# Kernel optimization log

Measured on AMD Instinct MI355X. Metric: run time of the kernel, lower is better.

## Reference

```python
import jax, jax.numpy as jnp
import numpy as np

L, D, H, DFF = 4, 1024, 16, 4096
DH = D // H
B, T = 2, 2048
EPS = 1e-5


def setup_inputs() -> dict:
    key = jax.random.key(0)
    ks = jax.random.split(key, 16)
    xav_a = (6.0 / (D + D)) ** 0.5      # xavier_uniform for square DxD
    xav_f1 = (6.0 / (D + DFF)) ** 0.5
    xav_f2 = (6.0 / (DFF + D)) ** 0.5
    def u(k, shape, a):
        return jax.random.uniform(k, shape, jnp.float32, -a, a)
    inp = {
        "x": jax.random.normal(ks[0], (B, T, D), jnp.float32),
        "mask": jnp.ones((B, T), jnp.int32),
        # attention projections, torch Linear layout [out, in]
        "Wq": u(ks[1], (L, D, D), xav_a), "bq": jnp.zeros((L, D), jnp.float32),
        "Wk": u(ks[2], (L, D, D), xav_a), "bk": jnp.zeros((L, D), jnp.float32),
        "Wv": u(ks[3], (L, D, D), xav_a), "bv": jnp.zeros((L, D), jnp.float32),
        "Wo": u(ks[4], (L, D, D), xav_a), "bo": jnp.zeros((L, D), jnp.float32),
        # FFN
        "fc1_w": u(ks[5], (L, DFF, D), xav_f1), "fc1_b": jnp.zeros((L, DFF), jnp.float32),
        "fc2_w": u(ks[6], (L, D, DFF), xav_f2), "fc2_b": jnp.zeros((L, D), jnp.float32),
        # LayerNorms
        "ln1_g": jnp.ones((L, D), jnp.float32), "ln1_b": jnp.zeros((L, D), jnp.float32),
        "ln2_g": jnp.ones((L, D), jnp.float32), "ln2_b": jnp.zeros((L, D), jnp.float32),
        "lnf_g": jnp.ones((D,), jnp.float32), "lnf_b": jnp.zeros((D,), jnp.float32),
    }
    return inp


def _layernorm(x, g, b):
    mu = jnp.mean(x, axis=-1, keepdims=True)
    var = jnp.mean(jnp.square(x - mu), axis=-1, keepdims=True)
    return (x - mu) * jax.lax.rsqrt(var + EPS) * g + b


def _encoder_forward(x, mask, Wq, bq, Wk, bk, Wv, bv, Wo, bo,
                     fc1_w, fc1_b, fc2_w, fc2_b,
                     ln1_g, ln1_b, ln2_g, ln2_b, lnf_g, lnf_b):
    keep = mask.astype(bool)[:, None, None, :]  # [B,1,1,Tk]
    scale = 1.0 / (DH ** 0.5)
    for l in range(L):
        # --- multi-head self-attention ---
        q = (jnp.einsum('btd,ed->bte', x, Wq[l]) + bq[l]).reshape(B, T, H, DH).transpose(0, 2, 1, 3)
        k = (jnp.einsum('btd,ed->bte', x, Wk[l]) + bk[l]).reshape(B, T, H, DH).transpose(0, 2, 1, 3)
        v = (jnp.einsum('btd,ed->bte', x, Wv[l]) + bv[l]).reshape(B, T, H, DH).transpose(0, 2, 1, 3)
        logits = jnp.einsum('bhqd,bhkd->bhqk', q, k) * scale
        logits = jnp.where(keep, logits, -jnp.inf)
        attn = jax.nn.softmax(logits, axis=-1)
        ctx = jnp.einsum('bhqk,bhkd->bhqd', attn, v).transpose(0, 2, 1, 3).reshape(B, T, D)
        attn_out = jnp.einsum('btd,ed->bte', ctx, Wo[l]) + bo[l]
        x = _layernorm(x + attn_out, ln1_g[l], ln1_b[l])
        # --- feed-forward (exact GELU, like torch nn.GELU default) ---
        h = jax.nn.gelu(jnp.einsum('btd,fd->btf', x, fc1_w[l]) + fc1_b[l], approximate=False)
        ff_out = jnp.einsum('btf,df->btd', h, fc2_w[l]) + fc2_b[l]
        x = _layernorm(x + ff_out, ln2_g[l], ln2_b[l])
    return _layernorm(x, lnf_g, lnf_b)


def reference(x, mask, Wq, bq, Wk, bk, Wv, bv, Wo, bo,
              fc1_w, fc1_b, fc2_w, fc2_b,
              ln1_g, ln1_b, ln2_g, ln2_b, lnf_g, lnf_b):
    return _encoder_forward(x, mask, Wq, bq, Wk, bk, Wv, bv, Wo, bo,
                            fc1_w, fc1_b, fc2_w, fc2_b,
                            ln1_g, ln1_b, ln2_g, ln2_b, lnf_g, lnf_b)
```

## Files before the change

kernel.cpp:

```cpp
#include <hip/hip_runtime.h>
#include <hip/hip_bf16.h>
#include <cstdint>

#define BB 2
#define TT 2048
#define DD 1024
#define HH 16
#define DHH 64
#define DFF 4096
#define LL 4
#define MM (BB*TT)
#define NT (TT/64)

typedef __attribute__((ext_vector_type(8))) short short8v;
typedef __attribute__((ext_vector_type(4))) short short4v;
typedef __attribute__((ext_vector_type(4))) float floatx4;

typedef __attribute__((address_space(3))) void lds_void;
typedef const __attribute__((address_space(1))) void glb_void;

__device__ __forceinline__ void gload_lds16(const void* g, void* l) {
  __builtin_amdgcn_global_load_lds((glb_void*)g, (lds_void*)l, 16, 0, 0);
}

__device__ __forceinline__ float bf2f(short s) {
  union { unsigned u; float f; } v; v.u = ((unsigned)(unsigned short)s) << 16; return v.f;
}
__device__ __forceinline__ short f2bf(float f) {
  union { float f; unsigned u; } v; v.f = f;
  unsigned r = (v.u + 0x7fffu + ((v.u >> 16) & 1u)) >> 16;
  return (short)r;
}
__device__ __forceinline__ unsigned pack2bf(float a, float b) {
  __hip_bfloat162 h = __float22bfloat162_rn(make_float2(a, b));
  return *reinterpret_cast<unsigned*>(&h);
}
__device__ __forceinline__ float fexp2(float x) {
  float r; asm("v_exp_f32 %0, %1" : "=v"(r) : "v"(x)); return r;
}
__device__ __forceinline__ float max3f(float a, float b, float c) {
  float r; asm("v_max3_f32 %0, %1, %2, %3" : "=v"(r) : "v"(a), "v"(b), "v"(c)); return r;
}
__device__ __forceinline__ float gelu_fast(float x) {
  const float u = x * x;
  const float w = fmaf(u, -0.10294537f, -2.302203f);
  const float t = fexp2(w * x);
  return x * __builtin_amdgcn_rcpf(1.f + t);
}

#define SCL2 0.18033688011112042f
__device__ __forceinline__ short8v scale8(short8v v) {
  short8v r;
#pragma unroll
  for (int i = 0; i < 8; ++i) r[i] = f2bf(bf2f(v[i]) * SCL2);
  return r;
}

#define SEG (DD*DD)
#define WTOT (4*SEG + 2*DFF*DD)
__global__ __launch_bounds__(256) void cast_layer(
    const float* __restrict__ wq, const float* __restrict__ wk,
    const float* __restrict__ wv, const float* __restrict__ wo,
    const float* __restrict__ f1, const float* __restrict__ f2,
    short* __restrict__ dst)
{
  const int i = (blockIdx.x * 256 + threadIdx.x) * 4;
  const float* src; int off;
  if      (i <     SEG) { src = wq; off = i; }
  else if (i < 2 * SEG) { src = wk; off = i - SEG; }
  else if (i < 3 * SEG) { src = wv; off = i - 2 * SEG; }
  else if (i < 4 * SEG) { src = wo; off = i - 3 * SEG; }
  else if (i < 4 * SEG + DFF * DD) { src = f1; off = i - 4 * SEG; }
  else { src = f2; off = i - 4 * SEG - DFF * DD; }
  const float4 v = *(const float4*)(src + off);
  short4v o; o[0] = f2bf(v.x); o[1] = f2bf(v.y); o[2] = f2bf(v.z); o[3] = f2bf(v.w);
  *(short4v*)(dst + i) = o;
}

template<int GELU, int QKV>
__global__ __launch_bounds__(512, 2) void gemm256(
    const short* __restrict__ A, const short* __restrict__ W,
    const float* __restrict__ b0, const float* __restrict__ b1,
    const float* __restrict__ b2, short* __restrict__ C,
    int M, int N, int K)
{
  __shared__ __align__(16) short lds[65536];
  const int t = threadIdx.x;
  const int lane = t & 63, wave = t >> 6;
  const int wm = wave >> 2, wn = wave & 3;
  const int l15 = lane & 15, lg = lane >> 4;

  const int nwg = gridDim.x * gridDim.y;
  const int bid0 = blockIdx.y * gridDim.x + blockIdx.x;
  const int q8 = nwg >> 3;
  const int lid = (bid0 & 7) * q8 + (bid0 >> 3);
  const int bx = lid % gridDim.x, by = lid / gridDim.x;

  const size_t abase = (size_t)by * 256 * K;
  const size_t wbase = (size_t)bx * 256 * K;

  floatx4 acc[8][4];
  floatx4 zero = {0.f, 0.f, 0.f, 0.f};
#pragma unroll
  for (int m = 0; m < 8; ++m)
#pragma unroll
    for (int n = 0; n < 4; ++n) acc[m][n] = zero;

#define STG_A(sl_, h_, u_) do {                                                \
    _Pragma("unroll")                                                          \
    for (int j_ = 0; j_ < 2; ++j_) {                                           \
      const int c_ = j_ * 512 + t, r_ = c_ >> 3;                               \
      const int kc_ = (c_ & 7) ^ (r_ & 7);                                     \
      gload_lds16(A + abase + (size_t)((h_) * 128 + r_) * K + (u_) * 64 + kc_ * 8, \
                  &lds[(sl_) * 16384 + (h_) * 8192 + (j_ * 512 + wave * 64) * 8]); \
    } } while (0)
#define STG_B(sl_, h_, u_) do {                                                \
    _Pragma("unroll")                                                          \
    for (int j_ = 0; j_ < 2; ++j_) {                                           \
      const int c_ = j_ * 512 + t, r_ = c_ >> 3;                               \
      const int kc_ = (c_ & 7) ^ (r_ & 7);                                     \
      gload_lds16(W + wbase + (size_t)((h_) * 128 + r_) * K + (u_) * 64 + kc_ * 8, \
                  &lds[32768 + (sl_) * 16384 + (h_) * 8192 + (j_ * 512 + wave * 64) * 8]); \
    } } while (0)

  const int NTK = K >> 6;
  STG_A(0, 0, 0); STG_A(0, 1, 0); STG_B(0, 0, 0); STG_B(0, 1, 0);

  for (int u = 0; u < NTK; ++u) {
    const int sl = u & 1, ns = sl ^ 1;
    const int aoff = sl * 16384 + wm * 8192;
    const int boff = 32768 + sl * 16384 + (wn >> 1) * 8192;
    short8v bfr[4][2];
#pragma unroll
    for (int p = 0; p < 4; ++p) {
      if (p == 0) {
        if (u + 1 < NTK) {
          STG_A(ns, 0, u + 1);
          asm volatile("s_waitcnt vmcnt(2)" ::: "memory");
        } else {
          asm volatile("s_waitcnt vmcnt(0)" ::: "memory");
        }
        __builtin_amdgcn_s_barrier();
#pragma unroll
        for (int n = 0; n < 4; ++n)
#pragma unroll
          for (int kk = 0; kk < 2; ++kk) {
            const int rl = (wn & 1) * 64 + n * 16 + l15;
            bfr[n][kk] = *(const short8v*)&lds[boff + rl * 64 + ((kk * 4 + lg) ^ (rl & 7)) * 8];
          }
      } else if (p == 1) { if (u + 1 < NTK) STG_A(ns, 1, u + 1); }
      else if (p == 2)   { if (u + 1 < NTK) STG_B(ns, 0, u + 1); }
      else               { if (u + 1 < NTK) STG_B(ns, 1, u + 1); }

      short8v af[2][2];
#pragma unroll
      for (int i = 0; i < 2; ++i)
#pragma unroll
        for (int kk = 0; kk < 2; ++kk) {
          const int rl = (2 * p + i) * 16 + l15;
          af[i][kk] = *(const short8v*)&lds[aoff + rl * 64 + ((kk * 4 + lg) ^ (rl & 7)) * 8];
        }
      asm volatile("s_waitcnt lgkmcnt(0)" ::: "memory");
      __builtin_amdgcn_s_setprio(1);
#pragma unroll
      for (int kk = 0; kk < 2; ++kk)
#pragma unroll
        for (int i = 0; i < 2; ++i)
#pragma unroll
          for (int n = 0; n < 4; ++n)
            acc[2 * p + i][n] = __builtin_amdgcn_mfma_f32_16x16x32_bf16(
                af[i][kk], bfr[n][kk], acc[2 * p + i][n], 0, 0, 0);
      __builtin_amdgcn_s_setprio(0);
      __builtin_amdgcn_s_barrier();
    }
  }
#undef STG_A
#undef STG_B

  const float* bp;
  int cbase = bx * 256 + wn * 64;
  if (QKV) {
    const int seg = cbase >> 10;
    bp = (seg == 0) ? b0 : (seg == 1 ? b1 : b2);
    cbase -= seg << 10;
  } else {
    bp = b0;
  }
  float bv[4];
#pragma unroll
  for (int n = 0; n < 4; ++n)
    bv[n] = bp[cbase + n * 16 + l15];
#pragma unroll
  for (int m = 0; m < 8; ++m)
#pragma unroll
    for (int jj = 0; jj < 4; ++jj) {
      const int row = by * 256 + wm * 128 + m * 16 + lg * 4 + jj;
      short* cp = C + (size_t)row * N + bx * 256 + wn * 64 + l15;
#pragma unroll
      for (int n = 0; n < 4; ++n) {
        float v = acc[m][n][jj] + bv[n];
        if (GELU) v = gelu_fast(v);
        cp[n * 16] = f2bf(v);
      }
    }
}

template<int GELU>
__global__ __launch_bounds__(512, 2) void gemm128(
    const short* __restrict__ A, const short* __restrict__ W,
    const float* __restrict__ bias, short* __restrict__ C,
    int M, int N, int K)
{
  __shared__ __align__(16) short lds[49152];
  const int t = threadIdx.x;
  const int lane = t & 63, wave = t >> 6;
  const int wm = wave >> 2, wn = wave & 3;
  const int l15 = lane & 15, lg = lane >> 4;

  const int nwg = gridDim.x * gridDim.y;
  const int bid0 = blockIdx.y * gridDim.x + blockIdx.x;
  const int q8 = nwg >> 3;
  const int lid = (bid0 & 7) * q8 + (bid0 >> 3);
  const int bx = lid % gridDim.x, by = lid / gridDim.x;

  const size_t abase = (size_t)by * 128 * K;
  const size_t wbase = (size_t)bx * 128 * K;

  floatx4 acc[4][2];
  floatx4 zero = {0.f, 0.f, 0.f, 0.f};
#pragma unroll
  for (int m = 0; m < 4; ++m)
#pragma unroll
    for (int n = 0; n < 2; ++n) acc[m][n] = zero;

#define STG128(sl_, u_) do {                                                   \
    _Pragma("unroll")                                                          \
    for (int j_ = 0; j_ < 2; ++j_) {                                           \
      const int c_ = j_ * 512 + t, r_ = c_ >> 3;                               \
      const int kc_ = (c_ & 7) ^ (r_ & 7);                                     \
      gload_lds16(A + abase + (size_t)r_ * K + (u_) * 64 + kc_ * 8,            \
                  &lds[(sl_) * 8192 + (j_ * 512 + wave * 64) * 8]);            \
      gload_lds16(W + wbase + (size_t)r_ * K + (u_) * 64 + kc_ * 8,            \
                  &lds[24576 + (sl_) * 8192 + (j_ * 512 + wave * 64) * 8]);    \
    } } while (0)

  const int NTK = K >> 6;
  STG128(0, 0);
  STG128(1, 1);

  for (int u = 0; u < NTK; ++u) {
    const int sl = u % 3;
    if (u + 1 < NTK) asm volatile("s_waitcnt vmcnt(4)" ::: "memory");
    else             asm volatile("s_waitcnt vmcnt(0)" ::: "memory");
    __builtin_amdgcn_s_barrier();
    if (u + 2 < NTK) STG128((u + 2) % 3, u + 2);

    short8v bfr[2][2], af[4][2];
#pragma unroll
    for (int n = 0; n < 2; ++n)
#pragma unroll
      for (int kk = 0; kk < 2; ++kk) {
        const int rl = wn * 32 + n * 16 + l15;
        bfr[n][kk] = *(const short8v*)&lds[24576 + sl * 8192 + rl * 64 + ((kk * 4 + lg) ^ (rl & 7)) * 8];
      }
#pragma unroll
    for (int m = 0; m < 4; ++m)
#pragma unroll
      for (int kk = 0; kk < 2; ++kk) {
        const int rl = wm * 32 + ((m & 1) * 16) + l15 + (m >> 1) * 64;
        af[m][kk] = *(const short8v*)&lds[sl * 8192 + rl * 64 + ((kk * 4 + lg) ^ (rl & 7)) * 8];
      }
    asm volatile("s_waitcnt lgkmcnt(0)" ::: "memory");
    __builtin_amdgcn_s_setprio(1);
#pragma unroll
    for (int kk = 0; kk < 2; ++kk)
#pragma unroll
      for (int m = 0; m < 4; ++m)
#pragma unroll
        for (int n = 0; n < 2; ++n)
          acc[m][n] = __builtin_amdgcn_mfma_f32_16x16x32_bf16(af[m][kk], bfr[n][kk], acc[m][n], 0, 0, 0);
    __builtin_amdgcn_s_setprio(0);
  }
#undef STG128

  float bv[2];
#pragma unroll
  for (int n = 0; n < 2; ++n)
    bv[n] = bias[bx * 128 + wn * 32 + n * 16 + l15];
#pragma unroll
  for (int m = 0; m < 4; ++m)
#pragma unroll
    for (int jj = 0; jj < 4; ++jj) {
      const int row = by * 128 + wm * 32 + (m & 1) * 16 + (m >> 1) * 64 + lg * 4 + jj;
      short* cp = C + (size_t)row * N + bx * 128 + wn * 32 + l15;
#pragma unroll
      for (int n = 0; n < 2; ++n) {
        float v = acc[m][n][jj] + bv[n];
        if (GELU) v = gelu_fast(v);
        cp[n * 16] = f2bf(v);
      }
    }
}

__global__ __launch_bounds__(256) void transpose_v(
    const short* __restrict__ qkv, short* __restrict__ vt)
{
  __shared__ short tile[64][65];
  const int tb = blockIdx.x, h = blockIdx.y, b = blockIdx.z;
  const int t = threadIdx.x;
  const int r = t >> 2, c4 = (t & 3) * 16;
  const short* src = qkv + ((size_t)(b * TT + tb * 64 + r)) * 3072 + 2048 + h * 64 + c4;
#pragma unroll
  for (int i = 0; i < 16; ++i) tile[r][c4 + i] = src[i];
  __syncthreads();
  short* dst = vt + ((size_t)((b * HH + h) * 64 + r)) * TT + tb * 64 + c4;
#pragma unroll
  for (int i = 0; i < 16; ++i) dst[i] = tile[c4 + i][r];
}

#define PSTR 72
__global__ __launch_bounds__(512, 4) void flash_attn(
    const short* __restrict__ qkv, const short* __restrict__ vt,
    const int* __restrict__ mask, short* __restrict__ ctx)
{
  const int t = threadIdx.x;
  const int lane = t & 63, wave = t >> 6;
  const int l15 = lane & 15, lg = lane >> 4;

  const int bid0 = blockIdx.x + gridDim.x * (blockIdx.y + gridDim.y * blockIdx.z);
  const int lid = (bid0 & 7) * 64 + (bid0 >> 3);
  const int qb = lid & 15, h = (lid >> 4) & 15, b = lid >> 8;

  __shared__ __align__(16) short Ks[3][64 * 64];
  __shared__ __align__(16) short Vs[3][64 * 64];
  __shared__ __align__(16) short p_lds[8][16 * PSTR];
  short* prow = p_lds[wave];

  const short* qp = qkv + ((size_t)(b * TT + qb * 128 + wave * 16 + l15)) * 3072 + h * 64;
  const short8v qf0 = scale8(*(const short8v*)(qp + lg * 8));
  const short8v qf1 = scale8(*(const short8v*)(qp + 32 + lg * 8));

  const short* kbase = qkv + (size_t)b * TT * 3072 + 1024 + h * 64;
  const short* vtb   = vt + ((size_t)(b * HH + h)) * 64 * TT;

  const int srow = lane >> 3;
  const int scol = (lane & 7) ^ (srow & 7);

  float m_run = -3e30f, l_run = 0.f;
  floatx4 zero = {0.f, 0.f, 0.f, 0.f};
  floatx4 o[4];
#pragma unroll
  for (int n = 0; n < 4; ++n) o[n] = zero;

#define STAGE_KV(bufi, kb_) do {                                             \
    const int r_ = wave * 8 + srow;                                          \
    gload_lds16(kbase + (size_t)((kb_) * 64 + r_) * 3072 + scol * 8,         \
                &Ks[bufi][wave * 512]);                                      \
    gload_lds16(vtb + (size_t)r_ * TT + (kb_) * 64 + scol * 8,               \
                &Vs[bufi][wave * 512]);                                      \
  } while (0)

  STAGE_KV(0, 0);
  STAGE_KV(1, 1);
  for (int kb = 0; kb < NT; ++kb) {
    const int sl = kb % 3;
    if (kb + 1 < NT) asm volatile("s_waitcnt vmcnt(2)" ::: "memory");
    else             asm volatile("s_waitcnt vmcnt(0)" ::: "memory");
    __builtin_amdgcn_s_barrier();
    if (kb + 2 < NT) STAGE_KV((kb + 2) % 3, kb + 2);

    float cm[4][4];
#pragma unroll
    for (int n = 0; n < 4; ++n) {
      const int4 mv = *(const int4*)&mask[b * TT + kb * 64 + n * 16 + lg * 4];
      cm[n][0] = mv.x ? 0.f : -1.5e30f; cm[n][1] = mv.y ? 0.f : -1.5e30f;
      cm[n][2] = mv.z ? 0.f : -1.5e30f; cm[n][3] = mv.w ? 0.f : -1.5e30f;
    }

    floatx4 s[4];
#pragma unroll
    for (int n = 0; n < 4; ++n) {
      const int row = n * 16 + l15;
      const int ch0 = lg ^ (row & 7);
      const int ch1 = (lg + 4) ^ (row & 7);
      const short8v kf0 = *(const short8v*)&Ks[sl][row * 64 + ch0 * 8];
      const short8v kf1 = *(const short8v*)&Ks[sl][row * 64 + ch1 * 8];
      floatx4 a = zero;
      a = __builtin_amdgcn_mfma_f32_16x16x32_bf16(kf0, qf0, a, 0, 0, 0);
      a = __builtin_amdgcn_mfma_f32_16x16x32_bf16(kf1, qf1, a, 0, 0, 0);
      s[n] = a;
    }
#pragma unroll
    for (int n = 0; n < 4; ++n)
#pragma unroll
      for (int jj = 0; jj < 4; ++jj) s[n][jj] += cm[n][jj];

    const float t0 = max3f(s[0][0], s[0][1], s[0][2]);
    const float t1 = max3f(s[0][3], s[1][0], s[1][1]);
    const float t2 = max3f(s[1][2], s[1][3], s[2][0]);
    const float t3 = max3f(s[2][1], s[2][2], s[2][3]);
    const float t4 = max3f(s[3][0], s[3][1], s[3][2]);
    float mx = fmaxf(max3f(t0, t1, t2), max3f(t3, t4, s[3][3]));
    mx = fmaxf(mx, __shfl_xor(mx, 16, 64));
    mx = fmaxf(mx, __shfl_xor(mx, 32, 64));

    const bool defer = __all(mx - m_run <= 11.5f);
    const float mnew = defer ? m_run : fmaxf(m_run, mx);
    float ps[4];
#pragma unroll
    for (int n = 0; n < 4; ++n) {
      s[n][0] = fexp2(s[n][0] - mnew);
      s[n][1] = fexp2(s[n][1] - mnew);
      s[n][2] = fexp2(s[n][2] - mnew);
      s[n][3] = fexp2(s[n][3] - mnew);
      ps[n] = (s[n][0] + s[n][1]) + (s[n][2] + s[n][3]);
    }
    float sum = (ps[0] + ps[1]) + (ps[2] + ps[3]);
    sum += __shfl_xor(sum, 16, 64);
    sum += __shfl_xor(sum, 32, 64);
    if (defer) {
      l_run += sum;
    } else {
      const float al = fexp2(m_run - mnew);
      l_run = l_run * al + sum;
      m_run = mnew;
      float alo[4];
#pragma unroll
      for (int jj = 0; jj < 4; ++jj) alo[jj] = __shfl(al, lg * 4 + jj, 16);
#pragma unroll
      for (int n = 0; n < 4; ++n)
#pragma unroll
        for (int jj = 0; jj < 4; ++jj) o[n][jj] *= alo[jj];
    }

#pragma unroll
    for (int n = 0; n < 4; ++n) {
      const unsigned u0 = pack2bf(s[n][0], s[n][1]);
      const unsigned u1 = pack2bf(s[n][2], s[n][3]);
      *(uint2*)&prow[l15 * PSTR + n * 16 + lg * 4] = make_uint2(u0, u1);
    }
    const short8v pf0 = *(const short8v*)&prow[l15 * PSTR + lg * 8];
    const short8v pf1 = *(const short8v*)&prow[l15 * PSTR + 32 + lg * 8];

#pragma unroll
    for (int n = 0; n < 4; ++n) {
      const int row = n * 16 + l15;
      const int ch0 = lg ^ (row & 7);
      const int ch1 = (lg + 4) ^ (row & 7);
      const short8v vf0 = *(const short8v*)&Vs[sl][row * 64 + ch0 * 8];
      const short8v vf1 = *(const short8v*)&Vs[sl][row * 64 + ch1 * 8];
      o[n] = __builtin_amdgcn_mfma_f32_16x16x32_bf16(pf0, vf0, o[n], 0, 0, 0);
      o[n] = __builtin_amdgcn_mfma_f32_16x16x32_bf16(pf1, vf1, o[n], 0, 0, 0);
    }
  }
#undef STAGE_KV

#pragma unroll
  for (int jj = 0; jj < 4; ++jj) {
    const float inv = 1.f / __shfl(l_run, lg * 4 + jj, 16);
    const int row = qb * 128 + wave * 16 + lg * 4 + jj;
#pragma unroll
    for (int n = 0; n < 4; ++n)
      ctx[((size_t)(b * TT + row)) * DD + h * 64 + n * 16 + l15] = f2bf(o[n][jj] * inv);
  }
}

__global__ __launch_bounds__(256) void add_ln(
    const float* __restrict__ xres, const short* __restrict__ add,
    const float* __restrict__ g, const float* __restrict__ bb,
    float* __restrict__ outf, short* __restrict__ outb)
{
  const int row = blockIdx.x, t = threadIdx.x;
  const int lane = t & 63, wave = t >> 6;
  const float4 xv = *(const float4*)(xres + (size_t)row * DD + t * 4);
  float y[4] = { xv.x, xv.y, xv.z, xv.w };
  if (add) {
    const short4v av = *(const short4v*)(add + (size_t)row * DD + t * 4);
#pragma unroll
    for (int i = 0; i < 4; ++i) y[i] += bf2f(av[i]);
  }
  float s = y[0] + y[1] + y[2] + y[3];
  float ss = y[0]*y[0] + y[1]*y[1] + y[2]*y[2] + y[3]*y[3];
#pragma unroll
  for (int off = 32; off >= 1; off >>= 1) {
    s  += __shfl_xor(s, off, 64);
    ss += __shfl_xor(ss, off, 64);
  }
  __shared__ float red[2][4];
  if (lane == 0) { red[0][wave] = s; red[1][wave] = ss; }
  __syncthreads();
  s  = red[0][0] + red[0][1] + red[0][2] + red[0][3];
  ss = red[1][0] + red[1][1] + red[1][2] + red[1][3];
  const float mu = s * (1.f / DD);
  const float var = ss * (1.f / DD) - mu * mu;
  const float rs = rsqrtf(var + 1e-5f);
  const float4 gv = *(const float4*)(g + t * 4);
  const float4 bv = *(const float4*)(bb + t * 4);
  float o[4];
  o[0] = (y[0] - mu) * rs * gv.x + bv.x;
  o[1] = (y[1] - mu) * rs * gv.y + bv.y;
  o[2] = (y[2] - mu) * rs * gv.z + bv.z;
  o[3] = (y[3] - mu) * rs * gv.w + bv.w;
  if (outf) *(float4*)(outf + (size_t)row * DD + t * 4) = make_float4(o[0], o[1], o[2], o[3]);
  if (outb) {
    short4v ov;
#pragma unroll
    for (int i = 0; i < 4; ++i) ov[i] = f2bf(o[i]);
    *(short4v*)(outb + (size_t)row * DD + t * 4) = ov;
  }
}

__global__ __launch_bounds__(256) void cast_in(
    const float* __restrict__ x, float* __restrict__ xf,
    short* __restrict__ xb)
{
  const int i = (blockIdx.x * 256 + threadIdx.x) * 4;
  const float4 v = *(const float4*)(x + i);
  *(float4*)(xf + i) = v;
  short4v o; o[0] = f2bf(v.x); o[1] = f2bf(v.y); o[2] = f2bf(v.z); o[3] = f2bf(v.w);
  *(short4v*)(xb + i) = o;
}

extern "C" void kernel_launch(void* const* d_in, const int* in_sizes, int n_in,
                              void* d_out, int out_size, void* d_ws, size_t ws_size,
                              hipStream_t stream) {
  const float* x   = (const float*)d_in[0];
  const int* mask  = (const int*)d_in[1];
  const float* Wq  = (const float*)d_in[2];
  const float* bq  = (const float*)d_in[3];
  const float* Wk  = (const float*)d_in[4];
  const float* bk  = (const float*)d_in[5];
  const float* Wv  = (const float*)d_in[6];
  const float* bv  = (const float*)d_in[7];
  const float* Wo  = (const float*)d_in[8];
  const float* bo  = (const float*)d_in[9];
  const float* f1w = (const float*)d_in[10];
  const float* f1b = (const float*)d_in[11];
  const float* f2w = (const float*)d_in[12];
  const float* f2b = (const float*)d_in[13];
  const float* l1g = (const float*)d_in[14];
  const float* l1b = (const float*)d_in[15];
  const float* l2g = (const float*)d_in[16];
  const float* l2b = (const float*)d_in[17];
  const float* lfg = (const float*)d_in[18];
  const float* lfb = (const float*)d_in[19];
  float* out = (float*)d_out;

  char* ws = (char*)d_ws;
  const size_t MB = 1u << 20;
  float* xf   = (float*)(ws);
  short* xb   = (short*)(ws + 16 * MB);
  short* qkv  = (short*)(ws + 24 * MB);
  short* vt_  = (short*)(ws + 48 * MB);
  short* ctx  = (short*)(ws + 56 * MB);
  short* tmp  = (short*)(ws + 64 * MB);
  short* wbuf = (short*)(ws + 72 * MB);
  short* hb   = qkv;

  cast_in<<<(MM * DD) / (256 * 4), 256, 0, stream>>>(x, xf, xb);

  for (int l = 0; l < LL; ++l) {
    cast_layer<<<WTOT / (256 * 4), 256, 0, stream>>>(
        Wq + (size_t)l * SEG, Wk + (size_t)l * SEG, Wv + (size_t)l * SEG, Wo + (size_t)l * SEG,
        f1w + (size_t)l * DFF * DD, f2w + (size_t)l * DD * DFF, wbuf);
    const short* wqkv_b = wbuf;
    const short* wo_b   = wbuf + 3 * SEG;
    const short* f1_b   = wbuf + 4 * SEG;
    const short* f2_b   = wbuf + 4 * SEG + DFF * DD;

    gemm256<0,1><<<dim3(3072 / 256, MM / 256), 512, 0, stream>>>(
        xb, wqkv_b, bq + l * DD, bk + l * DD, bv + l * DD, qkv, MM, 3072, DD);
    transpose_v<<<dim3(TT / 64, HH, BB), 256, 0, stream>>>(qkv, vt_);
    flash_attn<<<dim3(TT / 128, HH, BB), 512, 0, stream>>>(qkv, vt_, mask, ctx);
    gemm128<0><<<dim3(DD / 128, MM / 128), 512, 0, stream>>>(ctx, wo_b, bo + l * DD, tmp, MM, DD, DD);
    add_ln<<<MM, 256, 0, stream>>>(xf, tmp, l1g + l * DD, l1b + l * DD, xf, xb);
    gemm256<1,0><<<dim3(DFF / 256, MM / 256), 512, 0, stream>>>(
        xb, f1_b, f1b + l * DFF, nullptr, nullptr, hb, MM, DFF, DD);
    gemm128<0><<<dim3(DD / 128, MM / 128), 512, 0, stream>>>(hb, f2_b, f2b + l * DD, tmp, MM, DD, DFF);
    add_ln<<<MM, 256, 0, stream>>>(xf, tmp, l2g + l * DD, l2b + l * DD, xf, xb);
  }
  add_ln<<<MM, 256, 0, stream>>>(xf, nullptr, lfg, lfb, out, nullptr);
}
```

Measured before the change: 941.5 us.

## Load K and V fragments directly from global memory in flash attention

Removes the triple-buffered LDS staging of K and V tiles, along with its waitcnt and barrier synchronisation, in the flash attention kernel. Each wave now reads its MFMA K and V fragments straight from global memory and relies on the caches for reuse across the eight waves of a block. This cuts LDS usage and block-wide barriers, which may raise occupancy. The cost is redundant global and L2 traffic, since all waves fetch the same tiles, and no explicit prefetch overlap.

Measured after the change: 1.630 ms. 73.2% more time.

```diff
diff --git a/kernel.cpp b/kernel.cpp
--- a/kernel.cpp
+++ b/kernel.cpp
@@ -331,8 +331,6 @@
   const int lid = (bid0 & 7) * 64 + (bid0 >> 3);
   const int qb = lid & 15, h = (lid >> 4) & 15, b = lid >> 8;
 
-  __shared__ __align__(16) short Ks[3][64 * 64];
-  __shared__ __align__(16) short Vs[3][64 * 64];
   __shared__ __align__(16) short p_lds[8][16 * PSTR];
   short* prow = p_lds[wave];
 
@@ -340,11 +338,13 @@
   const short8v qf0 = scale8(*(const short8v*)(qp + lg * 8));
   const short8v qf1 = scale8(*(const short8v*)(qp + 32 + lg * 8));
 
-  const short* kbase = qkv + (size_t)b * TT * 3072 + 1024 + h * 64;
-  const short* vtb   = vt + ((size_t)(b * HH + h)) * 64 * TT;
-
-  const int srow = lane >> 3;
-  const int scol = (lane & 7) ^ (srow & 7);
+  const short* kr[4];
+  const short* vr[4];
+#pragma unroll
+  for (int n = 0; n < 4; ++n) {
+    kr[n] = qkv + (size_t)b * TT * 3072 + 1024 + h * 64 + (size_t)(n * 16 + l15) * 3072 + lg * 8;
+    vr[n] = vt + ((size_t)(b * HH + h)) * 64 * TT + (size_t)(n * 16 + l15) * TT + lg * 8;
+  }
 
   float m_run = -3e30f, l_run = 0.f;
   floatx4 zero = {0.f, 0.f, 0.f, 0.f};
@@ -352,23 +352,7 @@
 #pragma unroll
   for (int n = 0; n < 4; ++n) o[n] = zero;
 
-#define STAGE_KV(bufi, kb_) do {                                             \
-    const int r_ = wave * 8 + srow;                                          \
-    gload_lds16(kbase + (size_t)((kb_) * 64 + r_) * 3072 + scol * 8,         \
-                &Ks[bufi][wave * 512]);                                      \
-    gload_lds16(vtb + (size_t)r_ * TT + (kb_) * 64 + scol * 8,               \
-                &Vs[bufi][wave * 512]);                                      \
-  } while (0)
-
-  STAGE_KV(0, 0);
-  STAGE_KV(1, 1);
   for (int kb = 0; kb < NT; ++kb) {
-    const int sl = kb % 3;
-    if (kb + 1 < NT) asm volatile("s_waitcnt vmcnt(2)" ::: "memory");
-    else             asm volatile("s_waitcnt vmcnt(0)" ::: "memory");
-    __builtin_amdgcn_s_barrier();
-    if (kb + 2 < NT) STAGE_KV((kb + 2) % 3, kb + 2);
-
     float cm[4][4];
 #pragma unroll
     for (int n = 0; n < 4; ++n) {
@@ -380,11 +364,9 @@
     floatx4 s[4];
 #pragma unroll
     for (int n = 0; n < 4; ++n) {
-      const int row = n * 16 + l15;
-      const int ch0 = lg ^ (row & 7);
-      const int ch1 = (lg + 4) ^ (row & 7);
-      const short8v kf0 = *(const short8v*)&Ks[sl][row * 64 + ch0 * 8];
-      const short8v kf1 = *(const short8v*)&Ks[sl][row * 64 + ch1 * 8];
+      const short* kp = kr[n] + (size_t)kb * 64 * 3072;
+      const short8v kf0 = *(const short8v*)kp;
+      const short8v kf1 = *(const short8v*)(kp + 32);
       floatx4 a = zero;
       a = __builtin_amdgcn_mfma_f32_16x16x32_bf16(kf0, qf0, a, 0, 0, 0);
       a = __builtin_amdgcn_mfma_f32_16x16x32_bf16(kf1, qf1, a, 0, 0, 0);
@@ -444,16 +426,13 @@
 
 #pragma unroll
     for (int n = 0; n < 4; ++n) {
-      const int row = n * 16 + l15;
-      const int ch0 = lg ^ (row & 7);
-      const int ch1 = (lg + 4) ^ (row & 7);
-      const short8v vf0 = *(const short8v*)&Vs[sl][row * 64 + ch0 * 8];
-      const short8v vf1 = *(const short8v*)&Vs[sl][row * 64 + ch1 * 8];
+      const short* vp = vr[n] + kb * 64;
+      const short8v vf0 = *(const short8v*)vp;
+      const short8v vf1 = *(const short8v*)(vp + 32);
       o[n] = __builtin_amdgcn_mfma_f32_16x16x32_bf16(pf0, vf0, o[n], 0, 0, 0);
       o[n] = __builtin_amdgcn_mfma_f32_16x16x32_bf16(pf1, vf1, o[n], 0, 0, 0);
     }
   }
-#undef STAGE_KV
 
 #pragma unroll
   for (int jj = 0; jj < 4; ++jj) {
```
